# Performance work log

Hardware: AMD Instinct MI355X
Metric: run time of the kernel (lower is better)

Reference implementation:

```python
import jax, jax.numpy as jnp
import numpy as np

H = 16  # n_heads from init_kwargs


def setup_inputs() -> dict:
    key = jax.random.key(0)
    ks = jax.random.split(key, 9)
    B, N, D = 4, 4096, 1024
    mk = lambda k, shape: jax.random.normal(k, shape, dtype=jnp.float32) * 0.02
    return {
        "x": jax.random.normal(ks[0], (B, N, D), dtype=jnp.float32),
        "Wq": mk(ks[1], (D, D)), "bq": mk(ks[2], (D,)),
        "Wk": mk(ks[3], (D, D)), "bk": mk(ks[4], (D,)),
        "Wv": mk(ks[5], (D, D)), "bv": mk(ks[6], (D,)),
        "Wo": mk(ks[7], (D, D)), "bo": mk(ks[8], (D,)),
    }


def _split_heads(t):
    B, N, D = t.shape
    return t.reshape(B, N, H, D // H).transpose(0, 2, 1, 3)  # b h n d


def reference(x, Wq, bq, Wk, bk, Wv, bv, Wo, bo):
    B, N, D = x.shape
    d_head = D // H
    s = (d_head ** 0.5) ** (-0.25)
    q = _split_heads(x @ Wq + bq)
    # NOTE: original computes key(x) but immediately overwrites it with
    # q.softmax(dim=-2); key projection is dead code. We replicate exactly.
    _ = x @ Wk + bk  # dead, kept for parameter-shape parity
    v = _split_heads(x @ Wv + bv)
    q = jax.nn.softmax(q, axis=-1) * s            # softmax over d_head
    k = jax.nn.softmax(q, axis=-2) * s            # softmax of q over seq dim (faithful!)
    ctx = jnp.einsum('bhnd,bhne->bhde', k, v)     # k^T @ v, [B,H,d,d]
    attn = jnp.einsum('bhnd,bhde->bhne', q, ctx)  # q @ ctx, [B,H,N,d]
    attn = attn.transpose(0, 2, 1, 3).reshape(B, N, D)
    # n_heads > 1 -> to_out linear; dropout is identity in eval mode
    return attn @ Wo + bo
```

## Files before the change

kernel.cpp:

```cpp
#include <hip/hip_runtime.h>

typedef unsigned short u16;
typedef __attribute__((ext_vector_type(8))) short short8;
typedef __attribute__((ext_vector_type(4))) float f4;
typedef __attribute__((ext_vector_type(8))) unsigned short us8;

__device__ __forceinline__ u16 f2bf(float f) {
    unsigned u = __float_as_uint(f);
    u += 0x7FFFu + ((u >> 16) & 1u);
    return (u16)(u >> 16);
}
__device__ __forceinline__ float bf2f(u16 h) {
    return __uint_as_float(((unsigned)h) << 16);
}

#define GLD16(gp, lp) __builtin_amdgcn_global_load_lds( \
    (const __attribute__((address_space(1))) void*)(gp), \
    (__attribute__((address_space(3))) void*)(lp), 16, 0, 0)

#define SCALE_S 0.594603557501360533f

__global__ __launch_bounds__(256) void convert_f32_bf16(const float* __restrict__ in,
                                                        u16* __restrict__ out) {
    const size_t i = (size_t)blockIdx.x * 256 + threadIdx.x;
    const float4* p = (const float4*)in + i * 2;
    float4 a = p[0], b = p[1];
    us8 r;
    r[0] = f2bf(a.x); r[1] = f2bf(a.y); r[2] = f2bf(a.z); r[3] = f2bf(a.w);
    r[4] = f2bf(b.x); r[5] = f2bf(b.y); r[6] = f2bf(b.z); r[7] = f2bf(b.w);
    *(us8*)(out + i * 8) = r;
}

__global__ __launch_bounds__(256) void transpose_convert3(
    const float* __restrict__ Wq, const float* __restrict__ Wv, const float* __restrict__ Wo,
    u16* __restrict__ WqvT, u16* __restrict__ WoT) {
    const float* W; u16* out;
    if (blockIdx.z == 0)      { W = Wq; out = WqvT; }
    else if (blockIdx.z == 1) { W = Wv; out = WqvT + 1024 * 1024; }
    else                      { W = Wo; out = WoT; }
    __shared__ float tile[32][33];
    const int tx = threadIdx.x, ty = threadIdx.y;
    const int x = blockIdx.x * 32 + tx;
#pragma unroll
    for (int i = 0; i < 4; ++i) {
        const int y = blockIdx.y * 32 + ty + i * 8;
        tile[ty + i * 8][tx] = W[(size_t)y * 1024 + x];
    }
    __syncthreads();
#pragma unroll
    for (int i = 0; i < 4; ++i) {
        const int yo = blockIdx.x * 32 + ty + i * 8;
        const int xo = blockIdx.y * 32 + tx;
        out[(size_t)yo * 1024 + xo] = f2bf(tile[tx][ty + i * 8]);
    }
}

__global__ void concat_bias(const float* __restrict__ bq, const float* __restrict__ bv,
                            float* __restrict__ bqv) {
    const int i = blockIdx.x * 256 + threadIdx.x;
    bqv[i] = (i < 1024) ? bq[i] : bv[i - 1024];
}

__global__ __launch_bounds__(256) void gemm_bt(
    const u16* __restrict__ A, const u16* __restrict__ BT,
    const float* __restrict__ bias, float* __restrict__ C,
    u16* __restrict__ qsOut, u16* __restrict__ vOut,
    int N, int K, int mode,
    long long Ab, long long Bb, long long Cb)
{
    __shared__ u16 As[128 * 64];
    __shared__ u16 Bs[128 * 64];
    const int t = threadIdx.x;
    const int w = t >> 6, l = t & 63;
    const int quad = l >> 4, lrow = l & 15;
    const int z = blockIdx.z;
    A  += (size_t)z * Ab;
    BT += (size_t)z * Bb;

    const int nbx = gridDim.x;
    int bx = blockIdx.x, by = blockIdx.y;
    if ((nbx & 7) == 0) {
        const int id = blockIdx.x + nbx * blockIdx.y;
        const int xcd = id & 7, j = id >> 3;
        const int xs = nbx >> 3;
        bx = xcd * xs + (j % xs);
        by = j / xs;
    }
    const int m0 = bx * 128;
    const int n0 = by * 128;
    const int wm = (w & 1) * 64, wn = (w >> 1) * 64;

    const int srow = t >> 3;
    const int scol_l = (t & 7) * 8;
    const int scol_g = ((t & 7) ^ (srow & 7)) * 8;

    const u16* ap[4];
    const u16* bp[4];
    u16* al[4];
    u16* bl[4];
#pragma unroll
    for (int p = 0; p < 4; ++p) {
        ap[p] = A  + (size_t)(m0 + p * 32 + srow) * K + scol_g;
        bp[p] = BT + (size_t)(n0 + p * 32 + srow) * K + scol_g;
        al[p] = &As[(p * 32 + srow) * 64 + scol_l];
        bl[p] = &Bs[(p * 32 + srow) * 64 + scol_l];
    }

    f4 acc[4][4] = {};
    const int swz = (quad ^ (lrow & 7)) << 3;

    for (int it = K >> 6; it > 0; --it) {
#pragma unroll
        for (int p = 0; p < 4; ++p) {
            GLD16(ap[p], al[p]);
            GLD16(bp[p], bl[p]);
            ap[p] += 64; bp[p] += 64;
        }
        __syncthreads();
#pragma unroll
        for (int kk = 0; kk < 2; ++kk) {
            const int koff = swz ^ (kk << 5);
            short8 a[4], b[4];
#pragma unroll
            for (int i = 0; i < 4; ++i)
                a[i] = *(const short8*)&As[(wm + i * 16 + lrow) * 64 + koff];
#pragma unroll
            for (int j = 0; j < 4; ++j)
                b[j] = *(const short8*)&Bs[(wn + j * 16 + lrow) * 64 + koff];
#pragma unroll
            for (int i = 0; i < 4; ++i)
#pragma unroll
                for (int j = 0; j < 4; ++j)
                    acc[i][j] = __builtin_amdgcn_mfma_f32_16x16x32_bf16(a[i], b[j], acc[i][j], 0, 0, 0);
        }
        __syncthreads();
    }

    const int colb = n0 + wn + lrow;
    const float b0 = bias[colb], b1 = bias[colb + 16], b2 = bias[colb + 32], b3 = bias[colb + 48];

    if (mode == 0) {
        C += (size_t)z * Cb;
#pragma unroll
        for (int i = 0; i < 4; ++i) {
            const int rbase = m0 + wm + i * 16 + quad * 4;
#pragma unroll
            for (int r = 0; r < 4; ++r) {
                float* cp = C + (size_t)(rbase + r) * N + colb;
                cp[0]  = acc[i][0][r] + b0;
                cp[16] = acc[i][1][r] + b1;
                cp[32] = acc[i][2][r] + b2;
                cp[48] = acc[i][3][r] + b3;
            }
        }
    } else {
        const bool isQ = (n0 + wn) < (N >> 1);
#pragma unroll
        for (int i = 0; i < 4; ++i) {
            const int rbase = m0 + wm + i * 16 + quad * 4;
#pragma unroll
            for (int r = 0; r < 4; ++r) {
                float v0 = acc[i][0][r] + b0;
                float v1 = acc[i][1][r] + b1;
                float v2 = acc[i][2][r] + b2;
                float v3 = acc[i][3][r] + b3;
                if (isQ) {
                    float m = fmaxf(fmaxf(v0, v1), fmaxf(v2, v3));
                    m = fmaxf(m, __shfl_xor(m, 1));
                    m = fmaxf(m, __shfl_xor(m, 2));
                    m = fmaxf(m, __shfl_xor(m, 4));
                    m = fmaxf(m, __shfl_xor(m, 8));
                    float e0 = __expf(v0 - m), e1 = __expf(v1 - m);
                    float e2 = __expf(v2 - m), e3 = __expf(v3 - m);
                    float sm = e0 + e1 + e2 + e3;
                    sm += __shfl_xor(sm, 1);
                    sm += __shfl_xor(sm, 2);
                    sm += __shfl_xor(sm, 4);
                    sm += __shfl_xor(sm, 8);
                    const float inv = SCALE_S / sm;
                    u16* qp = qsOut + (size_t)(rbase + r) * 1024 + colb;
                    qp[0]  = f2bf(e0 * inv);
                    qp[16] = f2bf(e1 * inv);
                    qp[32] = f2bf(e2 * inv);
                    qp[48] = f2bf(e3 * inv);
                } else {
                    u16* vp = vOut + (size_t)(rbase + r) * 1024 + (colb - 1024);
                    vp[0]  = f2bf(v0);
                    vp[16] = f2bf(v1);
                    vp[32] = f2bf(v2);
                    vp[48] = f2bf(v3);
                }
            }
        }
    }
}

#define ZSTR 68
__global__ __launch_bounds__(256) void ctx_accum(
    const u16* __restrict__ qs, const u16* __restrict__ vb,
    float* __restrict__ Mpart, float* __restrict__ Zpart)
{
    __shared__ float ldsE[32][ZSTR];
    __shared__ float ldsV[32][ZSTR];
    const int t = threadIdx.x;
    const int g = blockIdx.x;
    const int split = blockIdx.y;
    const int b = g >> 4, h = g & 15;
    const int d = t & 63;
    const int e0 = (t >> 6) * 16;
    const int r = t >> 3, cb = t & 7;
    const size_t rowbase = ((size_t)b * 4096 + (size_t)split * 256) * 1024 + h * 64;

    float2 acc2[8] = {};
    float z8[8] = {};

    for (int chunk = 0; chunk < 256; chunk += 32) {
        const size_t gi = rowbase + (size_t)(chunk + r) * 1024 + cb * 8;
        us8 q8 = *(const us8*)(qs + gi);
        us8 v8 = *(const us8*)(vb + gi);
        float e[8], vv[8];
#pragma unroll
        for (int j2 = 0; j2 < 8; ++j2) {
            e[j2] = __expf(bf2f((u16)q8[j2]));
            z8[j2] += e[j2];
            vv[j2] = bf2f((u16)v8[j2]);
        }
        __syncthreads();
        *(float4*)&ldsE[r][cb * 8]     = *(float4*)&e[0];
        *(float4*)&ldsE[r][cb * 8 + 4] = *(float4*)&e[4];
        *(float4*)&ldsV[r][cb * 8]     = *(float4*)&vv[0];
        *(float4*)&ldsV[r][cb * 8 + 4] = *(float4*)&vv[4];
        __syncthreads();
#pragma unroll 8
        for (int rr = 0; rr < 32; ++rr) {
            const float ev = ldsE[rr][d];
            const float2* vp2 = (const float2*)&ldsV[rr][e0];
#pragma unroll
            for (int q = 0; q < 8; ++q) {
                float2 v2 = vp2[q];
                acc2[q].x += ev * v2.x;
                acc2[q].y += ev * v2.y;
            }
        }
    }

    __syncthreads();
    *(float4*)&ldsE[r][cb * 8]     = *(float4*)&z8[0];
    *(float4*)&ldsE[r][cb * 8 + 4] = *(float4*)&z8[4];
    __syncthreads();
    if (t < 64) {
        float zs = 0.f;
#pragma unroll
        for (int rr = 0; rr < 32; ++rr) zs += ldsE[rr][t];
        Zpart[((size_t)split * 64 + g) * 64 + t] = zs;
    }

    float* mp = Mpart + ((size_t)split * 64 + g) * 4096 + (size_t)d * 64 + e0;
    const float* af = (const float*)acc2;
    *(float4*)&mp[0]  = *(const float4*)&af[0];
    *(float4*)&mp[4]  = *(const float4*)&af[4];
    *(float4*)&mp[8]  = *(const float4*)&af[8];
    *(float4*)&mp[12] = *(const float4*)&af[12];
}

__global__ __launch_bounds__(256) void ctx_norm(const float* __restrict__ Mpart,
                                                const float* __restrict__ Zpart,
                                                float* __restrict__ ctx2) {
    const int g = blockIdx.x, t = threadIdx.x;
    __shared__ float rz[64];
    if (t < 64) {
        float zsum = 0.f;
#pragma unroll
        for (int s = 0; s < 16; ++s) zsum += Zpart[((size_t)s * 64 + g) * 64 + t];
        rz[t] = SCALE_S / zsum;
    }
    __syncthreads();
    for (int idx = t; idx < 4096; idx += 256) {
        float m = 0.f;
#pragma unroll
        for (int s = 0; s < 16; ++s) m += Mpart[((size_t)s * 64 + g) * 4096 + idx];
        ctx2[(size_t)g * 4096 + idx] = m * rz[idx >> 6];
    }
}

__global__ __launch_bounds__(256) void woprime(const float* __restrict__ ctx2,
                                               const u16* __restrict__ WoT,
                                               u16* __restrict__ WopT) {
    __shared__ float ctxT[64 * 65];
    __shared__ __align__(16) u16 wo[64 * 64];
    const int t = threadIdx.x;
    const int jt = blockIdx.x, h = blockIdx.y, b = blockIdx.z;
    const int g = b * 16 + h;
    for (int idx = t; idx < 4096; idx += 256) {
        const int d = idx >> 6, e = idx & 63;
        ctxT[e * 65 + d] = ctx2[(size_t)g * 4096 + idx];
    }
    const int j0 = jt * 64;
#pragma unroll
    for (int c = 0; c < 2; ++c) {
        const int ii = c * 256 + t;
        const int j = ii >> 3, c8 = ii & 7;
        *(us8*)&wo[j * 64 + c8 * 8] = *(const us8*)&WoT[(size_t)(j0 + j) * 1024 + h * 64 + c8 * 8];
    }
    __syncthreads();
    const int d = t & 63, w = t >> 6;
    float accj[16] = {};
    for (int eb = 0; eb < 8; ++eb) {
        float c8[8];
#pragma unroll
        for (int e = 0; e < 8; ++e) c8[e] = ctxT[(eb * 8 + e) * 65 + d];
#pragma unroll
        for (int jj = 0; jj < 16; ++jj) {
            us8 w8 = *(const us8*)&wo[(jj * 4 + w) * 64 + eb * 8];
#pragma unroll
            for (int e = 0; e < 8; ++e)
                accj[jj] += bf2f((u16)w8[e]) * c8[e];
        }
    }
#pragma unroll
    for (int jj = 0; jj < 16; ++jj)
        WopT[(size_t)b * 1048576 + (size_t)(j0 + jj * 4 + w) * 1024 + h * 64 + d] = f2bf(accj[jj]);
}

extern "C" void kernel_launch(void* const* d_in, const int* in_sizes, int n_in,
                              void* d_out, int out_size, void* d_ws, size_t ws_size,
                              hipStream_t stream)
{
    const float* x  = (const float*)d_in[0];
    const float* Wq = (const float*)d_in[1];
    const float* bq = (const float*)d_in[2];
    const float* Wv = (const float*)d_in[5];
    const float* bv = (const float*)d_in[6];
    const float* Wo = (const float*)d_in[7];
    const float* bo = (const float*)d_in[8];
    float* out = (float*)d_out;

    char* ws = (char*)d_ws;
    size_t o = 0;
    auto alloc = [&](size_t bytes) { char* p = ws + o; o = (o + bytes + 255) & ~(size_t)255; return p; };
    u16*   x_bf  = (u16*)  alloc(16384ull * 1024 * 2);
    u16*   WqvT  = (u16*)  alloc(2048ull * 1024 * 2);
    u16*   WoT   = (u16*)  alloc(1024ull * 1024 * 2);
    float* bqv   = (float*)alloc(2048ull * 4);
    u16*   qs    = (u16*)  alloc(16384ull * 1024 * 2);
    u16*   vbuf  = (u16*)  alloc(16384ull * 1024 * 2);
    float* Mpart = (float*)alloc(16ull * 64 * 4096 * 4);
    float* Zpart = (float*)alloc(16ull * 64 * 64 * 4);
    float* ctx2  = (float*)alloc(64ull * 4096 * 4);
    u16*   WopT  = (u16*)  alloc(4ull * 1024 * 1024 * 2);
    (void)ws_size; (void)in_sizes; (void)n_in; (void)out_size;

    convert_f32_bf16<<<8192, 256, 0, stream>>>(x, x_bf);
    transpose_convert3<<<dim3(32, 32, 3), dim3(32, 8), 0, stream>>>(Wq, Wv, Wo, WqvT, WoT);
    concat_bias<<<8, 256, 0, stream>>>(bq, bv, bqv);

    gemm_bt<<<dim3(128, 16, 1), 256, 0, stream>>>(x_bf, WqvT, bqv, nullptr, qs, vbuf,
                                                  2048, 1024, 1, 0, 0, 0);
    ctx_accum<<<dim3(64, 16), 256, 0, stream>>>(qs, vbuf, Mpart, Zpart);
    ctx_norm<<<64, 256, 0, stream>>>(Mpart, Zpart, ctx2);
    woprime<<<dim3(16, 16, 4), 256, 0, stream>>>(ctx2, WoT, WopT);
    gemm_bt<<<dim3(32, 8, 4), 256, 0, stream>>>(qs, WopT, bo, out, nullptr, nullptr,
                                                1024, 1024, 0,
                                                4096ll * 1024, 1024ll * 1024, 4096ll * 1024);
}
```

Measured before the change: 360.4 us.

## Compute per-head context accumulation with bf16 MFMA instead of scalar FMA

New measurement: 326.3 us. -9.5%, faster.

```diff
diff --git a/kernel.cpp b/kernel.cpp
--- a/kernel.cpp
+++ b/kernel.cpp
@@ -195,72 +195,82 @@
     }
 }
 
-#define ZSTR 68
-__global__ __launch_bounds__(256) void ctx_accum(
+__global__ __launch_bounds__(256) void ctx_mfma(
     const u16* __restrict__ qs, const u16* __restrict__ vb,
     float* __restrict__ Mpart, float* __restrict__ Zpart)
 {
-    __shared__ float ldsE[32][ZSTR];
-    __shared__ float ldsV[32][ZSTR];
+    __shared__ __align__(16) u16 Et[64 * 64];
+    __shared__ __align__(16) u16 Vt[64 * 64];
     const int t = threadIdx.x;
+    const int w = t >> 6, l = t & 63;
+    const int quad = l >> 4, lrow = l & 15;
     const int g = blockIdx.x;
     const int split = blockIdx.y;
     const int b = g >> 4, h = g & 15;
-    const int d = t & 63;
-    const int e0 = (t >> 6) * 16;
-    const int r = t >> 3, cb = t & 7;
-    const size_t rowbase = ((size_t)b * 4096 + (size_t)split * 256) * 1024 + h * 64;
-
-    float2 acc2[8] = {};
-    float z8[8] = {};
-
-    for (int chunk = 0; chunk < 256; chunk += 32) {
-        const size_t gi = rowbase + (size_t)(chunk + r) * 1024 + cb * 8;
-        us8 q8 = *(const us8*)(qs + gi);
-        us8 v8 = *(const us8*)(vb + gi);
-        float e[8], vv[8];
-#pragma unroll
-        for (int j2 = 0; j2 < 8; ++j2) {
-            e[j2] = __expf(bf2f((u16)q8[j2]));
-            z8[j2] += e[j2];
-            vv[j2] = bf2f((u16)v8[j2]);
+
+    const int n0 = (l & 31) * 2;
+    const int d0 = w * 16 + (l >> 5) * 8;
+    const size_t gbase = ((size_t)b * 4096 + (size_t)split * 256) * 1024 + h * 64 + d0;
+
+    f4 acc[4] = {};
+    float zl = 0.f;
+
+    for (int slab = 0; slab < 4; ++slab) {
+        const size_t ga = gbase + (size_t)(slab * 64 + n0) * 1024;
+        us8 q8a = *(const us8*)(qs + ga);
+        us8 q8b = *(const us8*)(qs + ga + 1024);
+        us8 v8a = *(const us8*)(vb + ga);
+        us8 v8b = *(const us8*)(vb + ga + 1024);
+        unsigned epk[8], vpk[8];
+#pragma unroll
+        for (int j = 0; j < 8; ++j) {
+            epk[j] = (unsigned)f2bf(__expf(bf2f((u16)q8a[j])))
+                   | ((unsigned)f2bf(__expf(bf2f((u16)q8b[j]))) << 16);
+            vpk[j] = (unsigned)(u16)v8a[j] | ((unsigned)(u16)v8b[j] << 16);
+        }
+        if (slab) __syncthreads();
+#pragma unroll
+        for (int j = 0; j < 8; ++j) {
+            const int d = d0 + j;
+            const int off = d * 64 + (((n0 >> 3) ^ (d & 7)) << 3) + (n0 & 7);
+            *(unsigned*)&Et[off] = epk[j];
+            *(unsigned*)&Vt[off] = vpk[j];
         }
         __syncthreads();
-        *(float4*)&ldsE[r][cb * 8]     = *(float4*)&e[0];
-        *(float4*)&ldsE[r][cb * 8 + 4] = *(float4*)&e[4];
-        *(float4*)&ldsV[r][cb * 8]     = *(float4*)&vv[0];
-        *(float4*)&ldsV[r][cb * 8 + 4] = *(float4*)&vv[4];
-        __syncthreads();
-#pragma unroll 8
-        for (int rr = 0; rr < 32; ++rr) {
-            const float ev = ldsE[rr][d];
-            const float2* vp2 = (const float2*)&ldsV[rr][e0];
-#pragma unroll
-            for (int q = 0; q < 8; ++q) {
-                float2 v2 = vp2[q];
-                acc2[q].x += ev * v2.x;
-                acc2[q].y += ev * v2.y;
-            }
-        }
-    }
-
-    __syncthreads();
-    *(float4*)&ldsE[r][cb * 8]     = *(float4*)&z8[0];
-    *(float4*)&ldsE[r][cb * 8 + 4] = *(float4*)&z8[4];
-    __syncthreads();
-    if (t < 64) {
-        float zs = 0.f;
-#pragma unroll
-        for (int rr = 0; rr < 32; ++rr) zs += ldsE[rr][t];
-        Zpart[((size_t)split * 64 + g) * 64 + t] = zs;
-    }
-
-    float* mp = Mpart + ((size_t)split * 64 + g) * 4096 + (size_t)d * 64 + e0;
-    const float* af = (const float*)acc2;
-    *(float4*)&mp[0]  = *(const float4*)&af[0];
-    *(float4*)&mp[4]  = *(const float4*)&af[4];
-    *(float4*)&mp[8]  = *(const float4*)&af[8];
-    *(float4*)&mp[12] = *(const float4*)&af[12];
+#pragma unroll
+        for (int kk = 0; kk < 2; ++kk) {
+            const int blk = ((kk * 4 + quad) ^ (lrow & 7)) << 3;
+            short8 a = *(const short8*)&Et[(w * 16 + lrow) * 64 + blk];
+            short8 bfr[4];
+#pragma unroll
+            for (int j = 0; j < 4; ++j)
+                bfr[j] = *(const short8*)&Vt[(j * 16 + lrow) * 64 + blk];
+#pragma unroll
+            for (int j = 0; j < 4; ++j)
+                acc[j] = __builtin_amdgcn_mfma_f32_16x16x32_bf16(a, bfr[j], acc[j], 0, 0, 0);
+        }
+        {
+            const int d = w * 16 + (l & 15);
+            const int jb = (l >> 4) * 2;
+            const short8 s0 = *(const short8*)&Et[d * 64 + ((jb ^ (d & 7)) << 3)];
+            const short8 s1 = *(const short8*)&Et[d * 64 + (((jb + 1) ^ (d & 7)) << 3)];
+#pragma unroll
+            for (int j = 0; j < 8; ++j)
+                zl += bf2f((u16)s0[j]) + bf2f((u16)s1[j]);
+        }
+    }
+
+    zl += __shfl_xor(zl, 16);
+    zl += __shfl_xor(zl, 32);
+    if (l < 16)
+        Zpart[((size_t)split * 64 + g) * 64 + w * 16 + l] = zl;
+
+    float* mp = Mpart + ((size_t)split * 64 + g) * 4096;
+#pragma unroll
+    for (int j = 0; j < 4; ++j)
+#pragma unroll
+        for (int r = 0; r < 4; ++r)
+            mp[(w * 16 + quad * 4 + r) * 64 + j * 16 + lrow] = acc[j][r];
 }
 
 __global__ __launch_bounds__(256) void ctx_norm(const float* __restrict__ Mpart,
@@ -344,10 +354,10 @@
     float* bqv   = (float*)alloc(2048ull * 4);
     u16*   qs    = (u16*)  alloc(16384ull * 1024 * 2);
     u16*   vbuf  = (u16*)  alloc(16384ull * 1024 * 2);
-    float* Mpart = (float*)alloc(16ull * 64 * 4096 * 4);
     float* Zpart = (float*)alloc(16ull * 64 * 64 * 4);
     float* ctx2  = (float*)alloc(64ull * 4096 * 4);
     u16*   WopT  = (u16*)  alloc(4ull * 1024 * 1024 * 2);
+    float* Mpart = (float*)x_bf;
     (void)ws_size; (void)in_sizes; (void)n_in; (void)out_size;
 
     convert_f32_bf16<<<8192, 256, 0, stream>>>(x, x_bf);
@@ -356,7 +366,7 @@
 
     gemm_bt<<<dim3(128, 16, 1), 256, 0, stream>>>(x_bf, WqvT, bqv, nullptr, qs, vbuf,
                                                   2048, 1024, 1, 0, 0, 0);
-    ctx_accum<<<dim3(64, 16), 256, 0, stream>>>(qs, vbuf, Mpart, Zpart);
+    ctx_mfma<<<dim3(64, 16), 256, 0, stream>>>(qs, vbuf, Mpart, Zpart);
     ctx_norm<<<64, 256, 0, stream>>>(Mpart, Zpart, ctx2);
     woprime<<<dim3(16, 16, 4), 256, 0, stream>>>(ctx2, WoT, WopT);
     gemm_bt<<<dim3(32, 8, 4), 256, 0, stream>>>(qs, WopT, bo, out, nullptr, nullptr,
```
